# Kernel optimization log

Hardware: AMD Instinct MI355X
Metric: run time of the kernel (lower is better)

The kernel has to match this reference:

```python
import jax, jax.numpy as jnp
import numpy as np

N = 50000
E = 800000
D = 128
L = 3
BN_EPS = 1e-5


def _bn(h, gamma, beta, mean, var):
    # eval-mode BatchNorm1d using running stats
    return (h - mean) * (gamma * jax.lax.rsqrt(var + BN_EPS)) + beta


def setup_inputs() -> dict:
    key = jax.random.key(0)
    ks = jax.random.split(key, 8)
    x = jax.random.normal(ks[0], (N, D), dtype=jnp.float32)
    edge_index = jax.random.randint(ks[1], (2, E), 0, N, dtype=jnp.int32)
    s = 1.0 / np.sqrt(D)
    W1 = jax.random.uniform(ks[2], (L, D, D), jnp.float32, -s, s)
    b1 = jax.random.uniform(ks[3], (L, D), jnp.float32, -s, s)
    W2 = jax.random.uniform(ks[4], (L, D, D), jnp.float32, -s, s)
    b2 = jax.random.uniform(ks[5], (L, D), jnp.float32, -s, s)
    # BN params: [L, 2, D] -> (inner mlp BN, outer BN) gamma/beta; running mean/var
    g = jnp.ones((L, 2, D), jnp.float32)
    be = jnp.zeros((L, 2, D), jnp.float32)
    rm = jax.random.normal(ks[6], (L, 2, D), dtype=jnp.float32) * 0.1
    rv = jax.random.uniform(ks[7], (L, 2, D), jnp.float32, 0.5, 1.5)
    return {"x": x, "edge_index": edge_index, "W1": W1, "b1": b1, "W2": W2,
            "b2": b2, "g": g, "be": be, "rm": rm, "rv": rv}


def reference(x, edge_index, W1, b1, W2, b2, g, be, rm, rv):
    src, dst = edge_index[0], edge_index[1]
    h = x
    for i in range(L):
        # GINConv (eps=0): (1+eps)*h + sum over in-neighbors
        agg = jax.ops.segment_sum(h[src], dst, num_segments=N)
        h = h + agg
        # mlp: Linear -> BN -> ReLU -> Linear
        h = jnp.maximum(_bn(h @ W1[i] + b1[i], g[i, 0], be[i, 0], rm[i, 0], rv[i, 0]), 0.0)
        h = h @ W2[i] + b2[i]
        # outer BN + ReLU (dropout is identity in eval)
        h = jnp.maximum(_bn(h, g[i, 1], be[i, 1], rm[i, 1], rv[i, 1]), 0.0)
    return h
```

## Files before the change

kernel.cpp:

```cpp
#include <hip/hip_runtime.h>
#include <stdint.h>

#define NN 50000
#define NE 800000
#define DD 128
#define NL 3
#define NB_E 200
#define EPB 4000
#define NBK 196
#define MH (NBK*NB_E)
#define LSTR 136

typedef __attribute__((ext_vector_type(8))) short short8;
typedef __attribute__((ext_vector_type(4))) float f32x4;

__device__ __forceinline__ float b2f(unsigned short u){
  union { unsigned int i; float f; } v; v.i = ((unsigned int)u) << 16; return v.f;
}
__device__ __forceinline__ unsigned short f2b(float f){
  union { float f; unsigned int i; } v; v.f = f;
  unsigned int r = 0x7FFFu + ((v.i >> 16) & 1u);
  return (unsigned short)((v.i + r) >> 16);
}

__global__ __launch_bounds__(256) void k_hist(const int* __restrict__ dst,
                                              int* __restrict__ blkhist){
  __shared__ int h[NBK];
  int t = threadIdx.x, b = blockIdx.x;
  for (int i = t; i < NBK; i += 256) h[i] = 0;
  __syncthreads();
  int e0 = b * EPB;
  for (int i = t; i < EPB; i += 256){
    int d = dst[e0 + i];
    atomicAdd(&h[d >> 8], 1);
  }
  __syncthreads();
  for (int i = t; i < NBK; i += 256) blkhist[i * NB_E + b] = h[i];
}

__global__ void k_scanA(const int* __restrict__ in, int* __restrict__ out,
                        int* __restrict__ bsum, int n){
  __shared__ int s[256];
  int t = threadIdx.x, i = blockIdx.x * 256 + t;
  int v = (i < n) ? in[i] : 0;
  s[t] = v; __syncthreads();
  for (int d = 1; d < 256; d <<= 1){
    int x = (t >= d) ? s[t - d] : 0;
    __syncthreads();
    s[t] += x;
    __syncthreads();
  }
  if (i < n) out[i] = s[t] - v;
  if (t == 255) bsum[blockIdx.x] = s[255];
}

__global__ void k_scanB(int* __restrict__ bsum, int nblk){
  __shared__ int s[256];
  int t = threadIdx.x;
  int v = (t < nblk) ? bsum[t] : 0;
  s[t] = v; __syncthreads();
  for (int d = 1; d < 256; d <<= 1){
    int x = (t >= d) ? s[t - d] : 0;
    __syncthreads();
    s[t] += x;
    __syncthreads();
  }
  if (t < nblk) bsum[t] = s[t] - v;
}

__global__ void k_scanC(int* __restrict__ out, const int* __restrict__ bsum, int n){
  int i = blockIdx.x * 256 + threadIdx.x;
  if (i < n) out[i] += bsum[blockIdx.x];
}

__global__ __launch_bounds__(256) void k_bin(const int* __restrict__ src,
    const int* __restrict__ dst, const int* __restrict__ pos,
    unsigned int* __restrict__ binned){
  __shared__ int cur[NBK];
  int t = threadIdx.x, b = blockIdx.x;
  for (int i = t; i < NBK; i += 256) cur[i] = pos[i * NB_E + b];
  __syncthreads();
  int e0 = b * EPB;
  for (int i = t; i < EPB; i += 256){
    int d = dst[e0 + i];
    int s = src[e0 + i];
    int p = atomicAdd(&cur[d >> 8], 1);
    binned[p] = ((unsigned int)d << 16) | (unsigned int)s;
  }
}

__global__ __launch_bounds__(256) void k_csr(const unsigned int* __restrict__ binned,
    const int* __restrict__ pos, int* __restrict__ offs, int* __restrict__ counts,
    int* __restrict__ csr_src){
  __shared__ int h[256], ex[256], cur[256];
  int t = threadIdx.x, b = blockIdx.x;
  int r0 = pos[b * NB_E];
  int r1 = (b == NBK - 1) ? NE : pos[(b + 1) * NB_E];
  h[t] = 0; __syncthreads();
  for (int i = r0 + t; i < r1; i += 256){
    unsigned int pv = binned[i];
    atomicAdd(&h[(pv >> 16) & 255], 1);
  }
  __syncthreads();
  int v = h[t];
  ex[t] = v; __syncthreads();
  for (int d = 1; d < 256; d <<= 1){
    int x = (t >= d) ? ex[t - d] : 0;
    __syncthreads();
    ex[t] += x;
    __syncthreads();
  }
  int base = r0 + ex[t] - v;
  cur[t] = base;
  int gd = b * 256 + t;
  if (gd < NN){ offs[gd] = base; counts[gd] = v; }
  __syncthreads();
  for (int i = r0 + t; i < r1; i += 256){
    unsigned int pv = binned[i];
    int dl = (pv >> 16) & 255;
    int s = pv & 0xFFFF;
    int p = atomicAdd(&cur[dl], 1);
    csr_src[p] = s;
  }
}

__global__ void k_prep_w(const float* __restrict__ W1, const float* __restrict__ W2,
    unsigned short* __restrict__ Wthi, unsigned short* __restrict__ Wtlo){
  int idx = blockIdx.x * 256 + threadIdx.x;
  int mat = idx >> 14;
  int rem = idx & 16383;
  int k = rem >> 7, j = rem & 127;
  int layer = mat >> 1, which = mat & 1;
  const float* srcW = which ? W2 : W1;
  float w = srcW[layer * 16384 + k * DD + j];
  unsigned short hi = f2b(w);
  Wthi[mat * 16384 + j * DD + k] = hi;
  Wtlo[mat * 16384 + j * DD + k] = f2b(w - b2f(hi));
}

__global__ void k_prep_bn(const float* __restrict__ b1, const float* __restrict__ b2,
    const float* __restrict__ g, const float* __restrict__ be,
    const float* __restrict__ rm, const float* __restrict__ rv,
    float* __restrict__ sc, float* __restrict__ sh){
  int idx = blockIdx.x * 256 + threadIdx.x;
  if (idx >= NL * 2 * DD) return;
  int j = idx & 127;
  int w = (idx >> 7) & 1;
  int l = idx >> 8;
  int p = (l * 2 + w) * DD + j;
  float s = g[p] * rsqrtf(rv[p] + 1e-5f);
  float bias = w ? b2[l * DD + j] : b1[l * DD + j];
  sc[p] = s;
  sh[p] = fmaf(bias - rm[p], s, be[p]);
}

__global__ void k_cvt(const float* __restrict__ x,
    unsigned short* __restrict__ hi, unsigned short* __restrict__ lo){
  int i = blockIdx.x * 256 + threadIdx.x;
  float4 a = ((const float4*)x)[2 * i];
  float4 b = ((const float4*)x)[2 * i + 1];
  float v[8] = {a.x, a.y, a.z, a.w, b.x, b.y, b.z, b.w};
  short8 h8, l8;
  #pragma unroll
  for (int c = 0; c < 8; ++c){
    unsigned short h = f2b(v[c]);
    h8[c] = (short)h; l8[c] = (short)f2b(v[c] - b2f(h));
  }
  ((short8*)hi)[i] = h8;
  ((short8*)lo)[i] = l8;
}

template<int LAST>
__global__ __launch_bounds__(256, 6) void k_layer(
    const unsigned short* __restrict__ Shi, const unsigned short* __restrict__ Slo,
    const int* __restrict__ offs, const int* __restrict__ counts,
    const int* __restrict__ csr_src,
    const unsigned short* __restrict__ W1h, const unsigned short* __restrict__ W1l,
    const unsigned short* __restrict__ W2h, const unsigned short* __restrict__ W2l,
    const float* __restrict__ sc1, const float* __restrict__ sh1,
    const float* __restrict__ sc2, const float* __restrict__ sh2,
    unsigned short* __restrict__ Ohi, unsigned short* __restrict__ Olo,
    float* __restrict__ Of)
{
  __shared__ __align__(16) char smem[2 * 32 * LSTR * 2];
  unsigned short* Ahi_s = (unsigned short*)smem;
  unsigned short* Alo_s = Ahi_s + 32 * LSTR;

  int t = threadIdx.x;
  int base = blockIdx.x * 32;

  {
    int row_l = t >> 3, p = t & 7;
    int row_g = base + row_l; if (row_g > NN - 1) row_g = NN - 1;
    const short8* H8 = (const short8*)Shi;
    const short8* L8 = (const short8*)Slo;
    float acc[16];
    short8 xh0 = H8[row_g * 16 + p * 2], xh1 = H8[row_g * 16 + p * 2 + 1];
    short8 xl0 = L8[row_g * 16 + p * 2], xl1 = L8[row_g * 16 + p * 2 + 1];
    #pragma unroll
    for (int c = 0; c < 8; ++c){
      acc[c]     = b2f((unsigned short)xh0[c]) + b2f((unsigned short)xl0[c]);
      acc[8 + c] = b2f((unsigned short)xh1[c]) + b2f((unsigned short)xl1[c]);
    }
    int e = offs[row_g];
    int end = e + counts[row_g];
    for (; e + 4 <= end; e += 4){
      int s0 = csr_src[e], s1 = csr_src[e + 1], s2 = csr_src[e + 2], s3 = csr_src[e + 3];
      short8 a0 = H8[s0 * 16 + p * 2], b0 = H8[s0 * 16 + p * 2 + 1];
      short8 a1 = H8[s1 * 16 + p * 2], b1 = H8[s1 * 16 + p * 2 + 1];
      short8 a2 = H8[s2 * 16 + p * 2], b2 = H8[s2 * 16 + p * 2 + 1];
      short8 a3 = H8[s3 * 16 + p * 2], b3 = H8[s3 * 16 + p * 2 + 1];
      #pragma unroll
      for (int c = 0; c < 8; ++c){
        acc[c]     += b2f((unsigned short)a0[c]) + b2f((unsigned short)a1[c])
                    + b2f((unsigned short)a2[c]) + b2f((unsigned short)a3[c]);
        acc[8 + c] += b2f((unsigned short)b0[c]) + b2f((unsigned short)b1[c])
                    + b2f((unsigned short)b2[c]) + b2f((unsigned short)b3[c]);
      }
    }
    for (; e < end; ++e){
      int s0 = csr_src[e];
      short8 a0 = H8[s0 * 16 + p * 2], b0 = H8[s0 * 16 + p * 2 + 1];
      #pragma unroll
      for (int c = 0; c < 8; ++c){
        acc[c]     += b2f((unsigned short)a0[c]);
        acc[8 + c] += b2f((unsigned short)b0[c]);
      }
    }
    short8 oh0, ol0, oh1, ol1;
    #pragma unroll
    for (int c = 0; c < 8; ++c){
      unsigned short h0 = f2b(acc[c]);
      oh0[c] = (short)h0; ol0[c] = (short)f2b(acc[c] - b2f(h0));
      unsigned short h1 = f2b(acc[8 + c]);
      oh1[c] = (short)h1; ol1[c] = (short)f2b(acc[8 + c] - b2f(h1));
    }
    *(short8*)&Ahi_s[row_l * LSTR + p * 16]     = oh0;
    *(short8*)&Ahi_s[row_l * LSTR + p * 16 + 8] = oh1;
    *(short8*)&Alo_s[row_l * LSTR + p * 16]     = ol0;
    *(short8*)&Alo_s[row_l * LSTR + p * 16 + 8] = ol1;
  }
  __syncthreads();

  int wave = t >> 6, lane = t & 63, l16 = lane & 15, q = lane >> 4;
  int r0 = (wave >> 1) * 16;
  int c0 = (wave & 1) * 64;
  const short8* B1H = (const short8*)W1h;
  const short8* B1L = (const short8*)W1l;
  const short8* B2H = (const short8*)W2h;
  const short8* B2L = (const short8*)W2l;

  f32x4 acc[4];
  #pragma unroll
  for (int ct = 0; ct < 4; ++ct) acc[ct] = (f32x4){0.f, 0.f, 0.f, 0.f};
  #pragma unroll
  for (int kc = 0; kc < 4; ++kc){
    short8 ah = *(const short8*)&Ahi_s[(r0 + l16) * LSTR + kc * 32 + q * 8];
    short8 al = *(const short8*)&Alo_s[(r0 + l16) * LSTR + kc * 32 + q * 8];
    #pragma unroll
    for (int ct = 0; ct < 4; ++ct){
      int wr = c0 + ct * 16 + l16;
      short8 bh = B1H[wr * 16 + kc * 4 + q];
      short8 bl = B1L[wr * 16 + kc * 4 + q];
      acc[ct] = __builtin_amdgcn_mfma_f32_16x16x32_bf16(ah, bh, acc[ct], 0, 0, 0);
      acc[ct] = __builtin_amdgcn_mfma_f32_16x16x32_bf16(ah, bl, acc[ct], 0, 0, 0);
      acc[ct] = __builtin_amdgcn_mfma_f32_16x16x32_bf16(al, bh, acc[ct], 0, 0, 0);
    }
  }
  __syncthreads();

  #pragma unroll
  for (int ct = 0; ct < 4; ++ct){
    int col = c0 + ct * 16 + l16;
    float s = sc1[col], b = sh1[col];
    #pragma unroll
    for (int r = 0; r < 4; ++r){
      int rl = r0 + q * 4 + r;
      float v = fmaxf(fmaf(acc[ct][r], s, b), 0.f);
      unsigned short h = f2b(v);
      Ahi_s[rl * LSTR + col] = h;
      Alo_s[rl * LSTR + col] = f2b(v - b2f(h));
    }
  }
  __syncthreads();

  f32x4 acc2[4];
  #pragma unroll
  for (int ct = 0; ct < 4; ++ct) acc2[ct] = (f32x4){0.f, 0.f, 0.f, 0.f};
  #pragma unroll
  for (int kc = 0; kc < 4; ++kc){
    short8 ah = *(const short8*)&Ahi_s[(r0 + l16) * LSTR + kc * 32 + q * 8];
    short8 al = *(const short8*)&Alo_s[(r0 + l16) * LSTR + kc * 32 + q * 8];
    #pragma unroll
    for (int ct = 0; ct < 4; ++ct){
      int wr = c0 + ct * 16 + l16;
      short8 bh = B2H[wr * 16 + kc * 4 + q];
      short8 bl = B2L[wr * 16 + kc * 4 + q];
      acc2[ct] = __builtin_amdgcn_mfma_f32_16x16x32_bf16(ah, bh, acc2[ct], 0, 0, 0);
      acc2[ct] = __builtin_amdgcn_mfma_f32_16x16x32_bf16(ah, bl, acc2[ct], 0, 0, 0);
      acc2[ct] = __builtin_amdgcn_mfma_f32_16x16x32_bf16(al, bh, acc2[ct], 0, 0, 0);
    }
  }
  __syncthreads();

  if (!LAST){
    #pragma unroll
    for (int ct = 0; ct < 4; ++ct){
      int col = c0 + ct * 16 + l16;
      float s = sc2[col], b = sh2[col];
      #pragma unroll
      for (int r = 0; r < 4; ++r){
        int rl = r0 + q * 4 + r;
        float v = fmaxf(fmaf(acc2[ct][r], s, b), 0.f);
        unsigned short h = f2b(v);
        Ahi_s[rl * LSTR + col] = h;
        Alo_s[rl * LSTR + col] = f2b(v - b2f(h));
      }
    }
    int rr = lane >> 3, ch = lane & 7;
    #pragma unroll
    for (int i = 0; i < 2; ++i){
      int rl = r0 + i * 8 + rr;
      int rg = base + rl;
      short8 vh = *(const short8*)&Ahi_s[rl * LSTR + c0 + ch * 8];
      short8 vl = *(const short8*)&Alo_s[rl * LSTR + c0 + ch * 8];
      if (rg < NN){
        *(short8*)&Ohi[rg * DD + c0 + ch * 8] = vh;
        *(short8*)&Olo[rg * DD + c0 + ch * 8] = vl;
      }
    }
  } else {
    float* Cf = (float*)smem;
    #pragma unroll
    for (int ct = 0; ct < 4; ++ct){
      int col = c0 + ct * 16 + l16;
      float s = sc2[col], b = sh2[col];
      #pragma unroll
      for (int r = 0; r < 4; ++r){
        int rl = r0 + q * 4 + r;
        Cf[rl * 132 + col] = fmaxf(fmaf(acc2[ct][r], s, b), 0.f);
      }
    }
    int rr = lane >> 4, cf = (lane & 15) * 4;
    #pragma unroll
    for (int i = 0; i < 4; ++i){
      int rl = r0 + i * 4 + rr;
      int rg = base + rl;
      float4 v = *(const float4*)&Cf[rl * 132 + c0 + cf];
      if (rg < NN) *(float4*)&Of[rg * DD + c0 + cf] = v;
    }
  }
}

extern "C" void kernel_launch(void* const* d_in, const int* in_sizes, int n_in,
                              void* d_out, int out_size, void* d_ws, size_t ws_size,
                              hipStream_t stream) {
  const float* x  = (const float*)d_in[0];
  const int* ei   = (const int*)d_in[1];
  const float* W1 = (const float*)d_in[2];
  const float* b1 = (const float*)d_in[3];
  const float* W2 = (const float*)d_in[4];
  const float* b2 = (const float*)d_in[5];
  const float* g  = (const float*)d_in[6];
  const float* be = (const float*)d_in[7];
  const float* rm = (const float*)d_in[8];
  const float* rv = (const float*)d_in[9];

  const int* src = ei;
  const int* dst = ei + NE;

  char* w = (char*)d_ws;
  const size_t HB = (size_t)NN * DD * sizeof(unsigned short);
  unsigned short* S0hi = (unsigned short*)w; w += HB;
  unsigned short* S0lo = (unsigned short*)w; w += HB;
  unsigned short* S1hi = (unsigned short*)w; w += HB;
  unsigned short* S1lo = (unsigned short*)w; w += HB;
  unsigned short* Wthi = (unsigned short*)w; w += 6 * 16384 * sizeof(unsigned short);
  unsigned short* Wtlo = (unsigned short*)w; w += 6 * 16384 * sizeof(unsigned short);
  float* scv = (float*)w; w += NL * 2 * DD * sizeof(float);
  float* shv = (float*)w; w += NL * 2 * DD * sizeof(float);
  int* counts  = (int*)w; w += 200192;
  int* offs    = (int*)w; w += 200192;
  int* blkhist = (int*)w; w += MH * sizeof(int);
  int* pos     = (int*)w; w += MH * sizeof(int);
  int* bsum    = (int*)w; w += 1024;
  unsigned int* binned = (unsigned int*)w; w += (size_t)NE * sizeof(unsigned int);
  int* csr_src = (int*)w; w += (size_t)NE * sizeof(int);

  const int SCAN_BLK = (MH + 255) / 256;
  k_hist<<<NB_E, 256, 0, stream>>>(dst, blkhist);
  k_scanA<<<SCAN_BLK, 256, 0, stream>>>(blkhist, pos, bsum, MH);
  k_scanB<<<1, 256, 0, stream>>>(bsum, SCAN_BLK);
  k_scanC<<<SCAN_BLK, 256, 0, stream>>>(pos, bsum, MH);
  k_bin<<<NB_E, 256, 0, stream>>>(src, dst, pos, binned);
  k_csr<<<NBK, 256, 0, stream>>>(binned, pos, offs, counts, csr_src);

  k_prep_w<<<384, 256, 0, stream>>>(W1, W2, Wthi, Wtlo);
  k_prep_bn<<<3, 256, 0, stream>>>(b1, b2, g, be, rm, rv, scv, shv);
  k_cvt<<<NN * DD / 8 / 256, 256, 0, stream>>>(x, S0hi, S0lo);

  const int LAYER_BLOCKS = (NN + 31) / 32;

  for (int i = 0; i < NL; ++i){
    const unsigned short* W1h = Wthi + (size_t)(i * 2 + 0) * 16384;
    const unsigned short* W1l = Wtlo + (size_t)(i * 2 + 0) * 16384;
    const unsigned short* W2h = Wthi + (size_t)(i * 2 + 1) * 16384;
    const unsigned short* W2l = Wtlo + (size_t)(i * 2 + 1) * 16384;
    const float* sc1 = scv + (size_t)(i * 2 + 0) * DD;
    const float* sh1 = shv + (size_t)(i * 2 + 0) * DD;
    const float* sc2 = scv + (size_t)(i * 2 + 1) * DD;
    const float* sh2 = shv + (size_t)(i * 2 + 1) * DD;

    const unsigned short* Ih = (i & 1) ? S1hi : S0hi;
    const unsigned short* Il = (i & 1) ? S1lo : S0lo;
    unsigned short* Oh = (i & 1) ? S0hi : S1hi;
    unsigned short* Ol = (i & 1) ? S0lo : S1lo;

    if (i == NL - 1){
      k_layer<1><<<LAYER_BLOCKS, 256, 0, stream>>>(Ih, Il, offs, counts, csr_src,
          W1h, W1l, W2h, W2l, sc1, sh1, sc2, sh2,
          (unsigned short*)nullptr, (unsigned short*)nullptr, (float*)d_out);
    } else {
      k_layer<0><<<LAYER_BLOCKS, 256, 0, stream>>>(Ih, Il, offs, counts, csr_src,
          W1h, W1l, W2h, W2l, sc1, sh1, sc2, sh2, Oh, Ol, (float*)nullptr);
    }
  }
}
```

Baseline: 373.7 us.

## Split fused aggregate+MLP layer kernel into separate gather and MLP kernels

Moves neighbor aggregation out of the fused layer kernel into a standalone gather kernel. It uses 16 lanes per row, each loading one short8, and unrolls the edge loop by 8. The MLP kernel now reads the aggregated hi/lo bf16 rows from a global buffer into LDS. The aim is to raise occupancy and memory-level parallelism for the irregular gather, separate from the register-heavy MFMA stage. The cost is an extra global write and read of the aggregated features per layer, plus another kernel launch.

```diff
diff --git a/kernel.cpp b/kernel.cpp
--- a/kernel.cpp
+++ b/kernel.cpp
@@ -170,11 +170,57 @@
   ((short8*)lo)[i] = l8;
 }
 
-template<int LAST>
-__global__ __launch_bounds__(256, 6) void k_layer(
+__global__ __launch_bounds__(256, 8) void k_agg(
     const unsigned short* __restrict__ Shi, const unsigned short* __restrict__ Slo,
     const int* __restrict__ offs, const int* __restrict__ counts,
     const int* __restrict__ csr_src,
+    unsigned short* __restrict__ Ahi, unsigned short* __restrict__ Alo){
+  int t = blockIdx.x * 256 + threadIdx.x;
+  int row = t >> 4;
+  int l = t & 15;
+  const short8* H = (const short8*)Shi;
+  const short8* L = (const short8*)Slo;
+  int idx = row * 16 + l;
+  short8 s_h = H[idx]; short8 s_l = L[idx];
+  float acc[8];
+  #pragma unroll
+  for (int i = 0; i < 8; ++i)
+    acc[i] = b2f((unsigned short)s_h[i]) + b2f((unsigned short)s_l[i]);
+
+  int e = offs[row];
+  int end = e + counts[row];
+  for (; e + 8 <= end; e += 8){
+    int i0 = csr_src[e],   i1 = csr_src[e+1], i2 = csr_src[e+2], i3 = csr_src[e+3];
+    int i4 = csr_src[e+4], i5 = csr_src[e+5], i6 = csr_src[e+6], i7 = csr_src[e+7];
+    short8 g0 = H[i0*16+l], g1 = H[i1*16+l], g2 = H[i2*16+l], g3 = H[i3*16+l];
+    short8 g4 = H[i4*16+l], g5 = H[i5*16+l], g6 = H[i6*16+l], g7 = H[i7*16+l];
+    #pragma unroll
+    for (int i = 0; i < 8; ++i){
+      acc[i] += (b2f((unsigned short)g0[i]) + b2f((unsigned short)g1[i]))
+              + (b2f((unsigned short)g2[i]) + b2f((unsigned short)g3[i]))
+              + (b2f((unsigned short)g4[i]) + b2f((unsigned short)g5[i]))
+              + (b2f((unsigned short)g6[i]) + b2f((unsigned short)g7[i]));
+    }
+  }
+  for (; e < end; ++e){
+    short8 g0 = H[csr_src[e]*16 + l];
+    #pragma unroll
+    for (int i = 0; i < 8; ++i) acc[i] += b2f((unsigned short)g0[i]);
+  }
+
+  short8 oh, ol;
+  #pragma unroll
+  for (int i = 0; i < 8; ++i){
+    unsigned short h = f2b(acc[i]);
+    oh[i] = (short)h; ol[i] = (short)f2b(acc[i] - b2f(h));
+  }
+  ((short8*)Ahi)[idx] = oh;
+  ((short8*)Alo)[idx] = ol;
+}
+
+template<int LAST>
+__global__ __launch_bounds__(256, 8) void k_mlp2(
+    const unsigned short* __restrict__ Ahi, const unsigned short* __restrict__ Alo,
     const unsigned short* __restrict__ W1h, const unsigned short* __restrict__ W1l,
     const unsigned short* __restrict__ W2h, const unsigned short* __restrict__ W2l,
     const float* __restrict__ sc1, const float* __restrict__ sh1,
@@ -190,55 +236,16 @@
   int base = blockIdx.x * 32;
 
   {
-    int row_l = t >> 3, p = t & 7;
-    int row_g = base + row_l; if (row_g > NN - 1) row_g = NN - 1;
-    const short8* H8 = (const short8*)Shi;
-    const short8* L8 = (const short8*)Slo;
-    float acc[16];
-    short8 xh0 = H8[row_g * 16 + p * 2], xh1 = H8[row_g * 16 + p * 2 + 1];
-    short8 xl0 = L8[row_g * 16 + p * 2], xl1 = L8[row_g * 16 + p * 2 + 1];
-    #pragma unroll
-    for (int c = 0; c < 8; ++c){
-      acc[c]     = b2f((unsigned short)xh0[c]) + b2f((unsigned short)xl0[c]);
-      acc[8 + c] = b2f((unsigned short)xh1[c]) + b2f((unsigned short)xl1[c]);
-    }
-    int e = offs[row_g];
-    int end = e + counts[row_g];
-    for (; e + 4 <= end; e += 4){
-      int s0 = csr_src[e], s1 = csr_src[e + 1], s2 = csr_src[e + 2], s3 = csr_src[e + 3];
-      short8 a0 = H8[s0 * 16 + p * 2], b0 = H8[s0 * 16 + p * 2 + 1];
-      short8 a1 = H8[s1 * 16 + p * 2], b1 = H8[s1 * 16 + p * 2 + 1];
-      short8 a2 = H8[s2 * 16 + p * 2], b2 = H8[s2 * 16 + p * 2 + 1];
-      short8 a3 = H8[s3 * 16 + p * 2], b3 = H8[s3 * 16 + p * 2 + 1];
-      #pragma unroll
-      for (int c = 0; c < 8; ++c){
-        acc[c]     += b2f((unsigned short)a0[c]) + b2f((unsigned short)a1[c])
-                    + b2f((unsigned short)a2[c]) + b2f((unsigned short)a3[c]);
-        acc[8 + c] += b2f((unsigned short)b0[c]) + b2f((unsigned short)b1[c])
-                    + b2f((unsigned short)b2[c]) + b2f((unsigned short)b3[c]);
-      }
-    }
-    for (; e < end; ++e){
-      int s0 = csr_src[e];
-      short8 a0 = H8[s0 * 16 + p * 2], b0 = H8[s0 * 16 + p * 2 + 1];
-      #pragma unroll
-      for (int c = 0; c < 8; ++c){
-        acc[c]     += b2f((unsigned short)a0[c]);
-        acc[8 + c] += b2f((unsigned short)b0[c]);
-      }
-    }
-    short8 oh0, ol0, oh1, ol1;
-    #pragma unroll
-    for (int c = 0; c < 8; ++c){
-      unsigned short h0 = f2b(acc[c]);
-      oh0[c] = (short)h0; ol0[c] = (short)f2b(acc[c] - b2f(h0));
-      unsigned short h1 = f2b(acc[8 + c]);
-      oh1[c] = (short)h1; ol1[c] = (short)f2b(acc[8 + c] - b2f(h1));
-    }
-    *(short8*)&Ahi_s[row_l * LSTR + p * 16]     = oh0;
-    *(short8*)&Ahi_s[row_l * LSTR + p * 16 + 8] = oh1;
-    *(short8*)&Alo_s[row_l * LSTR + p * 16]     = ol0;
-    *(short8*)&Alo_s[row_l * LSTR + p * 16 + 8] = ol1;
+    const short8* AH = (const short8*)Ahi;
+    const short8* AL = (const short8*)Alo;
+    #pragma unroll
+    for (int it = 0; it < 2; ++it){
+      int idx = it * 256 + t;
+      int rl = idx >> 4, ch = idx & 15;
+      int rg = base + rl; if (rg > NN - 1) rg = NN - 1;
+      *(short8*)&Ahi_s[rl * LSTR + ch * 8] = AH[rg * 16 + ch];
+      *(short8*)&Alo_s[rl * LSTR + ch * 8] = AL[rg * 16 + ch];
+    }
   }
   __syncthreads();
 
@@ -375,6 +382,8 @@
   unsigned short* S0lo = (unsigned short*)w; w += HB;
   unsigned short* S1hi = (unsigned short*)w; w += HB;
   unsigned short* S1lo = (unsigned short*)w; w += HB;
+  unsigned short* Ahi  = (unsigned short*)w; w += HB;
+  unsigned short* Alo  = (unsigned short*)w; w += HB;
   unsigned short* Wthi = (unsigned short*)w; w += 6 * 16384 * sizeof(unsigned short);
   unsigned short* Wtlo = (unsigned short*)w; w += 6 * 16384 * sizeof(unsigned short);
   float* scv = (float*)w; w += NL * 2 * DD * sizeof(float);
@@ -399,7 +408,8 @@
   k_prep_bn<<<3, 256, 0, stream>>>(b1, b2, g, be, rm, rv, scv, shv);
   k_cvt<<<NN * DD / 8 / 256, 256, 0, stream>>>(x, S0hi, S0lo);
 
-  const int LAYER_BLOCKS = (NN + 31) / 32;
+  const int AGG_BLOCKS = NN * 16 / 256;
+  const int MLP_BLOCKS = (NN + 31) / 32;
 
   for (int i = 0; i < NL; ++i){
     const unsigned short* W1h = Wthi + (size_t)(i * 2 + 0) * 16384;
@@ -416,12 +426,14 @@
     unsigned short* Oh = (i & 1) ? S0hi : S1hi;
     unsigned short* Ol = (i & 1) ? S0lo : S1lo;
 
+    k_agg<<<AGG_BLOCKS, 256, 0, stream>>>(Ih, Il, offs, counts, csr_src, Ahi, Alo);
+
     if (i == NL - 1){
-      k_layer<1><<<LAYER_BLOCKS, 256, 0, stream>>>(Ih, Il, offs, counts, csr_src,
+      k_mlp2<1><<<MLP_BLOCKS, 256, 0, stream>>>(Ahi, Alo,
           W1h, W1l, W2h, W2l, sc1, sh1, sc2, sh2,
           (unsigned short*)nullptr, (unsigned short*)nullptr, (float*)d_out);
     } else {
-      k_layer<0><<<LAYER_BLOCKS, 256, 0, stream>>>(Ih, Il, offs, counts, csr_src,
+      k_mlp2<0><<<MLP_BLOCKS, 256, 0, stream>>>(Ahi, Alo,
           W1h, W1l, W2h, W2l, sc1, sh1, sc2, sh2, Oh, Ol, (float*)nullptr);
     }
   }
```

Result: slower. 406.6 us (+8.8%).
